# Kernel optimization log

Hardware: AMD Instinct MI355X
Metric: run time of the kernel (lower is better)

The kernel has to match this reference:

```python
import jax, jax.numpy as jnp
import numpy as np

N = 8192   # nodes
F = 16     # node features (col 0 = signal, last 3 = xyz)
H = 64     # hidden
G = 256    # number of graphs (segments)
EPS = 1e-3 # keras LayerNormalization default epsilon


def setup_inputs() -> dict:
    key = jax.random.key(0)
    ks = jax.random.split(key, 10)
    s = 0.05
    X = jax.random.normal(ks[0], (N, F), jnp.float32)
    # dense pre-normalized adjacency (spektral GCNConv expects normalized A)
    A = jax.random.uniform(ks[1], (N, N), jnp.float32) * (1.0 / N)
    I = jnp.sort(jax.random.randint(ks[2], (N,), 0, G)).astype(jnp.int32)
    W0 = jax.random.normal(ks[3], (F, H), jnp.float32) * s
    b0 = jnp.zeros((H,), jnp.float32)
    g0 = jnp.ones((H,), jnp.float32)
    be0 = jnp.zeros((H,), jnp.float32)
    W1 = jax.random.normal(ks[4], (H, H), jnp.float32) * s
    b1 = jnp.zeros((H,), jnp.float32)
    g1 = jnp.ones((H,), jnp.float32)
    be1 = jnp.zeros((H,), jnp.float32)
    Wf = jax.random.normal(ks[5], (H, H), jnp.float32) * s
    bf = jnp.zeros((H,), jnp.float32)
    Wa = jax.random.normal(ks[6], (H, H), jnp.float32) * s
    ba = jnp.zeros((H,), jnp.float32)
    Wout = jax.random.normal(ks[7], (H + 3, 3), jnp.float32) * s
    bout = jnp.zeros((3,), jnp.float32)
    return dict(X=X, A=A, I=I, W0=W0, b0=b0, g0=g0, be0=be0,
                W1=W1, b1=b1, g1=g1, be1=be1,
                Wf=Wf, bf=bf, Wa=Wa, ba=ba, Wout=Wout, bout=bout)


def _layer_norm(x, gamma, beta):
    m = jnp.mean(x, axis=-1, keepdims=True)
    v = jnp.mean(jnp.square(x - m), axis=-1, keepdims=True)
    return (x - m) * jax.lax.rsqrt(v + EPS) * gamma + beta


def reference(X, A, I, W0, b0, g0, be0, W1, b1, g1, be1, Wf, bf, Wa, ba, Wout, bout):
    I = I.astype(jnp.int32)
    # GCN layer 0: relu(A @ X @ W0 + b0) -> LayerNorm
    h0 = _layer_norm(jax.nn.relu(A @ (X @ W0) + b0), g0, be0)
    # GCN layer 1 + LayerNorm + residual (i > 0)
    h = _layer_norm(jax.nn.relu(A @ (h0 @ W1) + b1), g1, be1) + h0
    # GlobalAttentionPool: Dense features * sigmoid-gated attention, segment-summed per graph
    feat = h @ Wf + bf                       # [N, H]
    attn = jax.nn.sigmoid(h @ Wa + ba)       # [N, H]
    g = jax.ops.segment_sum(feat * attn, I, num_segments=G)  # [G, H]
    # Signal-weighted barycentre via segment-softmax over log1p(relu(signal))
    z = jnp.log1p(jax.nn.relu(X[:, 0]))                       # [N]
    zmax = jax.ops.segment_max(z, I, num_segments=G)          # [G]
    zexp = jnp.exp(z - zmax[I])                               # [N]
    zsum = jax.ops.segment_sum(zexp, I, num_segments=G)       # [G]
    w = zexp / zsum[I]                                        # [N]
    bary = jax.ops.segment_sum(w[:, None] * X[:, -3:], I, num_segments=G)  # [G, 3]
    return jnp.concatenate([g, bary], axis=-1) @ Wout + bout  # [G, 3]
```

## Files before the change

kernel.cpp:

```cpp
#include <hip/hip_runtime.h>
#include <hip/hip_bf16.h>
#include <math.h>

#define NN 8192
#define FF 16
#define HH 64
#define GG 256
#define LN_EPS 1e-3f
#define KSPLIT 8
#define KC (NN / KSPLIT)

typedef __bf16 bf16x8 __attribute__((ext_vector_type(8)));
typedef float  floatx4 __attribute__((ext_vector_type(4)));

__global__ void k1_xw0(const float* __restrict__ X,
                       const float* __restrict__ W0,
                       const int* __restrict__ I,
                       __hip_bfloat16* __restrict__ Zt0,
                       float* __restrict__ zarr,
                       unsigned int* __restrict__ zmax_bits) {
    const int b = blockIdx.x, tid = threadIdx.x;
    const int lane = tid & 63;
    const int i = (b & 127) * 64 + lane;
    const int n = ((b >> 7) << 2) + (tid >> 6);
    float s = 0.f;
#pragma unroll
    for (int m = 0; m < FF; ++m)
        s += X[i * FF + m] * W0[m * HH + n];
    Zt0[(size_t)n * NN + i] = __float2bfloat16(s);

    if (b < 128 && tid < 64) {
        const int ii = b * 64 + lane;
        float z = log1pf(fmaxf(X[ii * FF], 0.f));
        zarr[ii] = z;
        atomicMax(&zmax_bits[I[ii]], __float_as_uint(z));
    }
}

__global__ __launch_bounds__(256)
void k_gemm_split(const float* __restrict__ A,
                  const __hip_bfloat16* __restrict__ Zt,
                  float* __restrict__ C) {
    const int tid  = threadIdx.x;
    const int wave = tid >> 6;
    const int lane = tid & 63;
    const int l16  = lane & 15;
    const int quad = lane >> 4;
    const int rb   = blockIdx.x & 127;
    const int kb   = blockIdx.x >> 7;
    const int row0 = rb * 64;
    const int k0   = kb * KC;

    const float* aptr = A + (size_t)(row0 + wave * 16 + l16) * NN + k0 + quad * 8;
    const __hip_bfloat16* bp0 = Zt + (size_t)(0 * 16 + l16) * NN + k0 + quad * 8;
    const __hip_bfloat16* bp1 = Zt + (size_t)(1 * 16 + l16) * NN + k0 + quad * 8;
    const __hip_bfloat16* bp2 = Zt + (size_t)(2 * 16 + l16) * NN + k0 + quad * 8;
    const __hip_bfloat16* bp3 = Zt + (size_t)(3 * 16 + l16) * NN + k0 + quad * 8;

    floatx4 acc0 = {0.f,0.f,0.f,0.f}, acc1 = {0.f,0.f,0.f,0.f};
    floatx4 acc2 = {0.f,0.f,0.f,0.f}, acc3 = {0.f,0.f,0.f,0.f};

#pragma unroll 4
    for (int k = 0; k < KC; k += 32) {
        const float4 a0 = *reinterpret_cast<const float4*>(aptr + k);
        const float4 a1 = *reinterpret_cast<const float4*>(aptr + k + 4);
        bf16x8 af;
        af[0] = (__bf16)a0.x; af[1] = (__bf16)a0.y;
        af[2] = (__bf16)a0.z; af[3] = (__bf16)a0.w;
        af[4] = (__bf16)a1.x; af[5] = (__bf16)a1.y;
        af[6] = (__bf16)a1.z; af[7] = (__bf16)a1.w;
        const bf16x8 b0 = *reinterpret_cast<const bf16x8*>(bp0 + k);
        const bf16x8 b1 = *reinterpret_cast<const bf16x8*>(bp1 + k);
        const bf16x8 b2 = *reinterpret_cast<const bf16x8*>(bp2 + k);
        const bf16x8 b3 = *reinterpret_cast<const bf16x8*>(bp3 + k);
        acc0 = __builtin_amdgcn_mfma_f32_16x16x32_bf16(af, b0, acc0, 0, 0, 0);
        acc1 = __builtin_amdgcn_mfma_f32_16x16x32_bf16(af, b1, acc1, 0, 0, 0);
        acc2 = __builtin_amdgcn_mfma_f32_16x16x32_bf16(af, b2, acc2, 0, 0, 0);
        acc3 = __builtin_amdgcn_mfma_f32_16x16x32_bf16(af, b3, acc3, 0, 0, 0);
    }

    const size_t rbase = (size_t)(row0 + wave * 16 + quad * 4);
#pragma unroll
    for (int r = 0; r < 4; ++r) {
        float* crow = C + (rbase + r) * HH + l16;
        atomicAdd(crow +  0, acc0[r]);
        atomicAdd(crow + 16, acc1[r]);
        atomicAdd(crow + 32, acc2[r]);
        atomicAdd(crow + 48, acc3[r]);
    }
}

__global__ __launch_bounds__(256)
void k_ln(const float* __restrict__ C,
          const float* __restrict__ bias,
          const float* __restrict__ gamma,
          const float* __restrict__ beta,
          const float* __restrict__ resid,
          float* __restrict__ out) {
    const int tid = threadIdx.x;
    const int row = tid >> 4;
    const int c0  = (tid & 15) * 4;
    const size_t grow = (size_t)(blockIdx.x * 16 + row);

    float4 v4 = *reinterpret_cast<const float4*>(&C[grow * HH + c0]);
    const float4 b4 = *reinterpret_cast<const float4*>(&bias[c0]);
    float v[4] = { fmaxf(v4.x + b4.x, 0.f), fmaxf(v4.y + b4.y, 0.f),
                   fmaxf(v4.z + b4.z, 0.f), fmaxf(v4.w + b4.w, 0.f) };
    float s = 0.f, ss = 0.f;
#pragma unroll
    for (int j = 0; j < 4; ++j) { s += v[j]; ss += v[j] * v[j]; }
#pragma unroll
    for (int m = 1; m < 16; m <<= 1) {
        s  += __shfl_xor(s,  m, 64);
        ss += __shfl_xor(ss, m, 64);
    }
    const float mean = s * (1.f / 64.f);
    const float var  = fmaxf(ss * (1.f / 64.f) - mean * mean, 0.f);
    const float inv  = rsqrtf(var + LN_EPS);
    const float4 g4  = *reinterpret_cast<const float4*>(&gamma[c0]);
    const float4 be4 = *reinterpret_cast<const float4*>(&beta[c0]);
    float4 o;
    o.x = (v[0] - mean) * inv * g4.x + be4.x;
    o.y = (v[1] - mean) * inv * g4.y + be4.y;
    o.z = (v[2] - mean) * inv * g4.z + be4.z;
    o.w = (v[3] - mean) * inv * g4.w + be4.w;
    if (resid) {
        const float4 r4 = *reinterpret_cast<const float4*>(&resid[grow * HH + c0]);
        o.x += r4.x; o.y += r4.y; o.z += r4.z; o.w += r4.w;
    }
    *reinterpret_cast<float4*>(&out[grow * HH + c0]) = o;
}

__global__ void k3_hw1(const float* __restrict__ h0,
                       const float* __restrict__ W1,
                       __hip_bfloat16* __restrict__ Zt1) {
    const int b = blockIdx.x, tid = threadIdx.x;
    const int lane = tid & 63;
    const int i = (b & 127) * 64 + lane;
    const int n = ((b >> 7) << 2) + (tid >> 6);
    float s = 0.f;
#pragma unroll 8
    for (int m = 0; m < HH; ++m)
        s += h0[(size_t)i * HH + m] * W1[m * HH + n];
    Zt1[(size_t)n * NN + i] = __float2bfloat16(s);
}

__global__ __launch_bounds__(256)
void k5_pool(const float* __restrict__ h,
             const float* __restrict__ Wf, const float* __restrict__ bfv,
             const float* __restrict__ Wa, const float* __restrict__ bav,
             const int* __restrict__ I,
             float* __restrict__ g) {
    __shared__ float hrow[4][64];
    const int w = threadIdx.x >> 6, l = threadIdx.x & 63;
    const int node = blockIdx.x * 4 + w;
    hrow[w][l] = h[(size_t)node * HH + l];
    __syncthreads();
    float sf = bfv[l], sa = bav[l];
#pragma unroll 8
    for (int m = 0; m < HH; ++m) {
        const float hv = hrow[w][m];
        sf += hv * Wf[m * HH + l];
        sa += hv * Wa[m * HH + l];
    }
    const float attn = 1.f / (1.f + expf(-sa));
    atomicAdd(&g[(size_t)I[node] * HH + l], sf * attn);
}

__global__ void k6_bary(const float* __restrict__ X,
                        const int* __restrict__ I,
                        const float* __restrict__ zarr,
                        const float* __restrict__ zmax,
                        float* __restrict__ zsum,
                        float* __restrict__ baryn) {
    const int i = blockIdx.x * 256 + threadIdx.x;
    const int seg = I[i];
    const float ze = expf(zarr[i] - zmax[seg]);
    atomicAdd(&zsum[seg], ze);
    atomicAdd(&baryn[seg * 3 + 0], ze * X[i * FF + 13]);
    atomicAdd(&baryn[seg * 3 + 1], ze * X[i * FF + 14]);
    atomicAdd(&baryn[seg * 3 + 2], ze * X[i * FF + 15]);
}

__global__ void k7_out(const float* __restrict__ g,
                       const float* __restrict__ zsum,
                       const float* __restrict__ baryn,
                       const float* __restrict__ Wout,
                       const float* __restrict__ bout,
                       float* __restrict__ out) {
    const int w = threadIdx.x >> 6, lane = threadIdx.x & 63;
    const int gi = blockIdx.x * 4 + w;
    const float vg = g[(size_t)gi * HH + lane];
    const float zs = zsum[gi];
    const float invz = (zs > 0.f) ? (1.f / zs) : 0.f;
    const float extra = (lane < 3) ? baryn[gi * 3 + lane] * invz : 0.f;
#pragma unroll
    for (int d = 0; d < 3; ++d) {
        float p = vg * Wout[lane * 3 + d];
        if (lane < 3) p += extra * Wout[(64 + lane) * 3 + d];
#pragma unroll
        for (int m = 1; m < 64; m <<= 1) p += __shfl_xor(p, m, 64);
        if (lane == 0) out[gi * 3 + d] = p + bout[d];
    }
}

extern "C" void kernel_launch(void* const* d_in, const int* in_sizes, int n_in,
                              void* d_out, int out_size, void* d_ws, size_t ws_size,
                              hipStream_t stream) {
    const float* X   = (const float*)d_in[0];
    const float* A   = (const float*)d_in[1];
    const int*   I   = (const int*)d_in[2];
    const float* W0  = (const float*)d_in[3];
    const float* b0  = (const float*)d_in[4];
    const float* g0  = (const float*)d_in[5];
    const float* be0 = (const float*)d_in[6];
    const float* W1  = (const float*)d_in[7];
    const float* b1  = (const float*)d_in[8];
    const float* g1  = (const float*)d_in[9];
    const float* be1 = (const float*)d_in[10];
    const float* Wf  = (const float*)d_in[11];
    const float* bfv = (const float*)d_in[12];
    const float* Wa  = (const float*)d_in[13];
    const float* bav = (const float*)d_in[14];
    const float* Wo  = (const float*)d_in[15];
    const float* bo  = (const float*)d_in[16];

    char* ws = (char*)d_ws;
    float* C0   = (float*)(ws);
    float* C1   = (float*)(ws + (2u << 20));
    float* accr = (float*)(ws + (4u << 20));
    float* g     = accr;
    float* zmax  = accr + GG * HH;
    float* zsum  = zmax + GG;
    float* baryn = zsum + GG;
    const size_t memset_bytes = (size_t)(2 * NN * HH + GG * HH + GG + GG + GG * 3) * sizeof(float);

    __hip_bfloat16* Zt0 = (__hip_bfloat16*)(ws + (4u << 20) + (128u << 10));
    __hip_bfloat16* Zt1 = (__hip_bfloat16*)(ws + (5u << 20) + (128u << 10));
    float* h0   = (float*)(ws + (6u << 20) + (128u << 10));
    float* h    = (float*)(ws + (8u << 20) + (128u << 10));
    float* zarr = (float*)(ws + (10u << 20) + (128u << 10));

    hipMemsetAsync(ws, 0, memset_bytes, stream);

    k1_xw0<<<2048, 256, 0, stream>>>(X, W0, I, Zt0, zarr, (unsigned int*)zmax);
    k_gemm_split<<<1024, 256, 0, stream>>>(A, Zt0, C0);
    k_ln<<<512, 256, 0, stream>>>(C0, b0, g0, be0, nullptr, h0);
    k3_hw1<<<2048, 256, 0, stream>>>(h0, W1, Zt1);
    k_gemm_split<<<1024, 256, 0, stream>>>(A, Zt1, C1);
    k_ln<<<512, 256, 0, stream>>>(C1, b1, g1, be1, h0, h);
    k5_pool<<<2048, 256, 0, stream>>>(h, Wf, bfv, Wa, bav, I, g);
    k6_bary<<<32, 256, 0, stream>>>(X, I, zarr, zmax, zsum, baryn);
    k7_out<<<64, 256, 0, stream>>>(g, zsum, baryn, Wo, bo, (float*)d_out);
}
```

Measured before the change: 602.0 us.

## Replace split-K atomics with partial buffers reduced in LayerNorm, double KSPLIT

The split-K GEMM now writes each K-slice's partial result to its own buffer instead of using float atomicAdd, and the LayerNorm kernel sums the KSPLIT partials before applying bias, ReLU and normalisation. KSPLIT goes from 8 to 16, doubling the grid to 2048 blocks for more parallelism over the 8192x8192 A matrix. The inner loop is software-pipelined so the next A and Z loads are issued before the current MFMAs, and the large memset of the C buffers is dropped. The trade is 16 partial buffers of 2 MB each to write and read back, in exchange for removing atomic contention.

New measurement: 638.1 us. 1.06x slower.

```diff
diff --git a/kernel.cpp b/kernel.cpp
--- a/kernel.cpp
+++ b/kernel.cpp
@@ -7,11 +7,18 @@
 #define HH 64
 #define GG 256
 #define LN_EPS 1e-3f
-#define KSPLIT 8
+#define KSPLIT 16
 #define KC (NN / KSPLIT)
 
 typedef __bf16 bf16x8 __attribute__((ext_vector_type(8)));
 typedef float  floatx4 __attribute__((ext_vector_type(4)));
+
+__device__ __forceinline__ bf16x8 cvt_bf8(const float4 a0, const float4 a1) {
+    bf16x8 r;
+    r[0] = (__bf16)a0.x; r[1] = (__bf16)a0.y; r[2] = (__bf16)a0.z; r[3] = (__bf16)a0.w;
+    r[4] = (__bf16)a1.x; r[5] = (__bf16)a1.y; r[6] = (__bf16)a1.z; r[7] = (__bf16)a1.w;
+    return r;
+}
 
 __global__ void k1_xw0(const float* __restrict__ X,
                        const float* __restrict__ W0,
@@ -40,7 +47,7 @@
 __global__ __launch_bounds__(256)
 void k_gemm_split(const float* __restrict__ A,
                   const __hip_bfloat16* __restrict__ Zt,
-                  float* __restrict__ C) {
+                  float* __restrict__ Cpart) {
     const int tid  = threadIdx.x;
     const int wave = tid >> 6;
     const int lane = tid & 63;
@@ -60,38 +67,52 @@
     floatx4 acc0 = {0.f,0.f,0.f,0.f}, acc1 = {0.f,0.f,0.f,0.f};
     floatx4 acc2 = {0.f,0.f,0.f,0.f}, acc3 = {0.f,0.f,0.f,0.f};
 
-#pragma unroll 4
-    for (int k = 0; k < KC; k += 32) {
-        const float4 a0 = *reinterpret_cast<const float4*>(aptr + k);
-        const float4 a1 = *reinterpret_cast<const float4*>(aptr + k + 4);
-        bf16x8 af;
-        af[0] = (__bf16)a0.x; af[1] = (__bf16)a0.y;
-        af[2] = (__bf16)a0.z; af[3] = (__bf16)a0.w;
-        af[4] = (__bf16)a1.x; af[5] = (__bf16)a1.y;
-        af[6] = (__bf16)a1.z; af[7] = (__bf16)a1.w;
-        const bf16x8 b0 = *reinterpret_cast<const bf16x8*>(bp0 + k);
-        const bf16x8 b1 = *reinterpret_cast<const bf16x8*>(bp1 + k);
-        const bf16x8 b2 = *reinterpret_cast<const bf16x8*>(bp2 + k);
-        const bf16x8 b3 = *reinterpret_cast<const bf16x8*>(bp3 + k);
-        acc0 = __builtin_amdgcn_mfma_f32_16x16x32_bf16(af, b0, acc0, 0, 0, 0);
-        acc1 = __builtin_amdgcn_mfma_f32_16x16x32_bf16(af, b1, acc1, 0, 0, 0);
-        acc2 = __builtin_amdgcn_mfma_f32_16x16x32_bf16(af, b2, acc2, 0, 0, 0);
-        acc3 = __builtin_amdgcn_mfma_f32_16x16x32_bf16(af, b3, acc3, 0, 0, 0);
-    }
-
+    float4 ca0 = *reinterpret_cast<const float4*>(aptr);
+    float4 ca1 = *reinterpret_cast<const float4*>(aptr + 4);
+    bf16x8 cb0 = *reinterpret_cast<const bf16x8*>(bp0);
+    bf16x8 cb1 = *reinterpret_cast<const bf16x8*>(bp1);
+    bf16x8 cb2 = *reinterpret_cast<const bf16x8*>(bp2);
+    bf16x8 cb3 = *reinterpret_cast<const bf16x8*>(bp3);
+
+#pragma unroll
+    for (int k = 32; k < KC; k += 32) {
+        const float4 na0 = *reinterpret_cast<const float4*>(aptr + k);
+        const float4 na1 = *reinterpret_cast<const float4*>(aptr + k + 4);
+        const bf16x8 nb0 = *reinterpret_cast<const bf16x8*>(bp0 + k);
+        const bf16x8 nb1 = *reinterpret_cast<const bf16x8*>(bp1 + k);
+        const bf16x8 nb2 = *reinterpret_cast<const bf16x8*>(bp2 + k);
+        const bf16x8 nb3 = *reinterpret_cast<const bf16x8*>(bp3 + k);
+
+        const bf16x8 af = cvt_bf8(ca0, ca1);
+        acc0 = __builtin_amdgcn_mfma_f32_16x16x32_bf16(af, cb0, acc0, 0, 0, 0);
+        acc1 = __builtin_amdgcn_mfma_f32_16x16x32_bf16(af, cb1, acc1, 0, 0, 0);
+        acc2 = __builtin_amdgcn_mfma_f32_16x16x32_bf16(af, cb2, acc2, 0, 0, 0);
+        acc3 = __builtin_amdgcn_mfma_f32_16x16x32_bf16(af, cb3, acc3, 0, 0, 0);
+
+        ca0 = na0; ca1 = na1; cb0 = nb0; cb1 = nb1; cb2 = nb2; cb3 = nb3;
+    }
+    {
+        const bf16x8 af = cvt_bf8(ca0, ca1);
+        acc0 = __builtin_amdgcn_mfma_f32_16x16x32_bf16(af, cb0, acc0, 0, 0, 0);
+        acc1 = __builtin_amdgcn_mfma_f32_16x16x32_bf16(af, cb1, acc1, 0, 0, 0);
+        acc2 = __builtin_amdgcn_mfma_f32_16x16x32_bf16(af, cb2, acc2, 0, 0, 0);
+        acc3 = __builtin_amdgcn_mfma_f32_16x16x32_bf16(af, cb3, acc3, 0, 0, 0);
+    }
+
+    float* Cp = Cpart + (size_t)kb * NN * HH;
     const size_t rbase = (size_t)(row0 + wave * 16 + quad * 4);
 #pragma unroll
     for (int r = 0; r < 4; ++r) {
-        float* crow = C + (rbase + r) * HH + l16;
-        atomicAdd(crow +  0, acc0[r]);
-        atomicAdd(crow + 16, acc1[r]);
-        atomicAdd(crow + 32, acc2[r]);
-        atomicAdd(crow + 48, acc3[r]);
+        float* crow = Cp + (rbase + r) * HH + l16;
+        crow[ 0] = acc0[r];
+        crow[16] = acc1[r];
+        crow[32] = acc2[r];
+        crow[48] = acc3[r];
     }
 }
 
 __global__ __launch_bounds__(256)
-void k_ln(const float* __restrict__ C,
+void k_ln(const float* __restrict__ Cpart,
           const float* __restrict__ bias,
           const float* __restrict__ gamma,
           const float* __restrict__ beta,
@@ -102,7 +123,13 @@
     const int c0  = (tid & 15) * 4;
     const size_t grow = (size_t)(blockIdx.x * 16 + row);
 
-    float4 v4 = *reinterpret_cast<const float4*>(&C[grow * HH + c0]);
+    float4 v4 = {0.f, 0.f, 0.f, 0.f};
+#pragma unroll
+    for (int s = 0; s < KSPLIT; ++s) {
+        const float4 p = *reinterpret_cast<const float4*>(
+            &Cpart[(size_t)s * NN * HH + grow * HH + c0]);
+        v4.x += p.x; v4.y += p.y; v4.z += p.z; v4.w += p.w;
+    }
     const float4 b4 = *reinterpret_cast<const float4*>(&bias[c0]);
     float v[4] = { fmaxf(v4.x + b4.x, 0.f), fmaxf(v4.y + b4.y, 0.f),
                    fmaxf(v4.z + b4.z, 0.f), fmaxf(v4.w + b4.w, 0.f) };
@@ -226,29 +253,28 @@
     const float* bo  = (const float*)d_in[16];
 
     char* ws = (char*)d_ws;
-    float* C0   = (float*)(ws);
-    float* C1   = (float*)(ws + (2u << 20));
-    float* accr = (float*)(ws + (4u << 20));
+    float* accr  = (float*)(ws);
     float* g     = accr;
     float* zmax  = accr + GG * HH;
     float* zsum  = zmax + GG;
     float* baryn = zsum + GG;
-    const size_t memset_bytes = (size_t)(2 * NN * HH + GG * HH + GG + GG + GG * 3) * sizeof(float);
-
-    __hip_bfloat16* Zt0 = (__hip_bfloat16*)(ws + (4u << 20) + (128u << 10));
-    __hip_bfloat16* Zt1 = (__hip_bfloat16*)(ws + (5u << 20) + (128u << 10));
-    float* h0   = (float*)(ws + (6u << 20) + (128u << 10));
-    float* h    = (float*)(ws + (8u << 20) + (128u << 10));
-    float* zarr = (float*)(ws + (10u << 20) + (128u << 10));
-
-    hipMemsetAsync(ws, 0, memset_bytes, stream);
+    const size_t memset_bytes = (size_t)(GG * HH + GG + GG + GG * 3) * sizeof(float);
+
+    __hip_bfloat16* Zt0 = (__hip_bfloat16*)(ws + (1u << 20));
+    __hip_bfloat16* Zt1 = (__hip_bfloat16*)(ws + (2u << 20));
+    float* h0    = (float*)(ws + (3u << 20));
+    float* h     = (float*)(ws + (5u << 20));
+    float* zarr  = (float*)(ws + (7u << 20));
+    float* Cpart = (float*)(ws + (8u << 20));
+
+    hipMemsetAsync(accr, 0, memset_bytes, stream);
 
     k1_xw0<<<2048, 256, 0, stream>>>(X, W0, I, Zt0, zarr, (unsigned int*)zmax);
-    k_gemm_split<<<1024, 256, 0, stream>>>(A, Zt0, C0);
-    k_ln<<<512, 256, 0, stream>>>(C0, b0, g0, be0, nullptr, h0);
+    k_gemm_split<<<2048, 256, 0, stream>>>(A, Zt0, Cpart);
+    k_ln<<<512, 256, 0, stream>>>(Cpart, b0, g0, be0, nullptr, h0);
     k3_hw1<<<2048, 256, 0, stream>>>(h0, W1, Zt1);
-    k_gemm_split<<<1024, 256, 0, stream>>>(A, Zt1, C1);
-    k_ln<<<512, 256, 0, stream>>>(C1, b1, g1, be1, h0, h);
+    k_gemm_split<<<2048, 256, 0, stream>>>(A, Zt1, Cpart);
+    k_ln<<<512, 256, 0, stream>>>(Cpart, b1, g1, be1, h0, h);
     k5_pool<<<2048, 256, 0, stream>>>(h, Wf, bfv, Wa, bav, I, g);
     k6_bary<<<32, 256, 0, stream>>>(X, I, zarr, zmax, zsum, baryn);
     k7_out<<<64, 256, 0, stream>>>(g, zsum, baryn, Wo, bo, (float*)d_out);
```
